# Kernel tuning notes

Measured on AMD Instinct MI355X. Metric: run time of the kernel, lower is better.

## Reference

```python
import jax, jax.numpy as jnp
import numpy as np

D_MODEL = 128
D_STATE = 16
D_CONV = 4
EXPAND = 2
D_INNER = EXPAND * D_MODEL        # 256
DT_RANK = (D_MODEL + 15) // 16    # 8


def setup_inputs() -> dict:
    key = jax.random.key(0)
    ks = jax.random.split(key, 12)
    bsz, dd, hh, ww = 2, 8, 32, 32
    x = jax.random.normal(ks[0], (bsz, D_MODEL, dd, hh, ww), dtype=jnp.float32)
    # LayerNorm params
    ln_w = jnp.ones((D_MODEL,), jnp.float32)
    ln_b = jnp.zeros((D_MODEL,), jnp.float32)
    # Mamba params (fan-in scaled random init)
    W_in = jax.random.normal(ks[1], (2 * D_INNER, D_MODEL), jnp.float32) / np.sqrt(D_MODEL)
    conv_w = jax.random.normal(ks[2], (D_INNER, D_CONV), jnp.float32) / np.sqrt(D_CONV)
    conv_b = jnp.zeros((D_INNER,), jnp.float32)
    W_x = jax.random.normal(ks[3], (DT_RANK + 2 * D_STATE, D_INNER), jnp.float32) / np.sqrt(D_INNER)
    W_dt = jax.random.normal(ks[4], (D_INNER, DT_RANK), jnp.float32) / np.sqrt(DT_RANK)
    # bias so softplus(dt) starts small, as in mamba's dt init
    b_dt = jnp.log(jnp.expm1(jax.random.uniform(ks[5], (D_INNER,), jnp.float32, 1e-3, 0.1)))
    # A_log = log(1..d_state) broadcast over channels (S4D-real init)
    A_log = jnp.log(jnp.broadcast_to(jnp.arange(1, D_STATE + 1, dtype=jnp.float32), (D_INNER, D_STATE)))
    D = jnp.ones((D_INNER,), jnp.float32)
    W_out = jax.random.normal(ks[6], (D_MODEL, D_INNER), jnp.float32) / np.sqrt(D_INNER)
    return {"x": x, "ln_w": ln_w, "ln_b": ln_b, "W_in": W_in, "conv_w": conv_w,
            "conv_b": conv_b, "W_x": W_x, "W_dt": W_dt, "b_dt": b_dt,
            "A_log": A_log, "D": D, "W_out": W_out}


def _mamba_layer(x, ln_w, ln_b, W_in, conv_w, conv_b, W_x, W_dt, b_dt, A_log, D, W_out):
    bsz, c, dd, hh, ww = x.shape
    L = dd * hh * ww
    xs = x.transpose(0, 2, 3, 4, 1).reshape(bsz, L, c)          # (b, L, d_model)
    # LayerNorm
    mu = xs.mean(-1, keepdims=True)
    var = ((xs - mu) ** 2).mean(-1, keepdims=True)
    xn = (xs - mu) * jax.lax.rsqrt(var + 1e-5) * ln_w + ln_b
    # in_proj -> x, z
    xz = jnp.einsum('blc,ec->ble', xn, W_in)                     # (b, L, 2*d_inner)
    xi, z = xz[..., :D_INNER], xz[..., D_INNER:]
    # causal depthwise conv1d + silu
    xi_t = xi.transpose(0, 2, 1)                                  # (b, d_inner, L)
    xc = jax.lax.conv_general_dilated(
        xi_t, conv_w[:, None, :], window_strides=(1,),
        padding=[(D_CONV - 1, 0)], feature_group_count=D_INNER)
    xc = jax.nn.silu(xc + conv_b[None, :, None]).transpose(0, 2, 1)  # (b, L, d_inner)
    # x_proj -> dt, B, C
    dbl = jnp.einsum('bld,ed->ble', xc, W_x)
    dt = dbl[..., :DT_RANK]
    Bm = dbl[..., DT_RANK:DT_RANK + D_STATE]                      # (b, L, n)
    Cm = dbl[..., DT_RANK + D_STATE:]                             # (b, L, n)
    dt = jax.nn.softplus(jnp.einsum('blr,dr->bld', dt, W_dt) + b_dt)  # (b, L, d_inner)
    A = -jnp.exp(A_log)                                           # (d_inner, n)
    dA = jnp.exp(jnp.einsum('bld,dn->bldn', dt, A))               # (b, L, d_inner, n)
    dBx = jnp.einsum('bln,bld->bldn', Bm, dt * xc)                # (b, L, d_inner, n)

    def step(h, inp):
        dA_t, dBx_t, C_t = inp
        h = dA_t * h + dBx_t                                      # (b, d_inner, n)
        y = jnp.einsum('bdn,bn->bd', h, C_t)
        return h, y

    h0 = jnp.zeros((bsz, D_INNER, D_STATE), xc.dtype)
    _, ys = jax.lax.scan(step, h0,
                         (dA.transpose(1, 0, 2, 3), dBx.transpose(1, 0, 2, 3), Cm.transpose(1, 0, 2)))
    y = ys.transpose(1, 0, 2) + xc * D                            # (b, L, d_inner)
    y = y * jax.nn.silu(z)
    out = jnp.einsum('bld,cd->blc', y, W_out)                     # (b, L, d_model)
    return out.reshape(bsz, dd, hh, ww, c).transpose(0, 4, 1, 2, 3)


def reference(x, ln_w, ln_b, W_in, conv_w, conv_b, W_x, W_dt, b_dt, A_log, D, W_out):
    return _mamba_layer(x, ln_w, ln_b, W_in, conv_w, conv_b, W_x, W_dt, b_dt, A_log, D, W_out)
```

## Files before the change

### kernel.cpp

```cpp
#include <hip/hip_runtime.h>

constexpr int kB  = 2;
constexpr int kL  = 8192;
constexpr int kC  = 128;
constexpr int kE  = 256;
constexpr int kN  = 16;
constexpr int kCL = 64;
constexpr int kNC = kL / kCL;

typedef __attribute__((ext_vector_type(8))) short bf16x8;
typedef __attribute__((ext_vector_type(4))) float f32x4;
typedef __attribute__((ext_vector_type(8))) unsigned short u16x8;

__device__ __forceinline__ float silu(float v) { return v / (1.f + __expf(-v)); }
__device__ __forceinline__ float softplusf(float s) {
  return fmaxf(s, 0.f) + log1pf(__expf(-fabsf(s)));
}
__device__ __forceinline__ unsigned short f2bf(float x) {
  unsigned u = __float_as_uint(x);
  u += 0x7FFF + ((u >> 16) & 1);
  return (unsigned short)(u >> 16);
}
__device__ __forceinline__ float bf2f(unsigned short x) {
  return __uint_as_float(((unsigned)x) << 16);
}
__device__ __forceinline__ float dpp_red8(float v) {
  v += __int_as_float(__builtin_amdgcn_mov_dpp(__float_as_int(v), 0xB1, 0xF, 0xF, true));
  v += __int_as_float(__builtin_amdgcn_mov_dpp(__float_as_int(v), 0x4E, 0xF, 0xF, true));
  v += __int_as_float(__builtin_amdgcn_mov_dpp(__float_as_int(v), 0x141, 0xF, 0xF, true));
  return v;
}

__global__ __launch_bounds__(256) void k_pre(const float* __restrict__ W_in,
                                             const float* __restrict__ W_x,
                                             const float* __restrict__ W_dt,
                                             const float* __restrict__ W_out,
                                             unsigned short* __restrict__ WinF,
                                             unsigned short* __restrict__ WcatF,
                                             unsigned short* __restrict__ WoutF,
                                             const float* __restrict__ x,
                                             const float* __restrict__ ln_w,
                                             const float* __restrict__ ln_b,
                                             unsigned short* __restrict__ xnH) {
  const int tid = threadIdx.x;
  if (blockIdx.x < 84) {
    const int f = blockIdx.x * 256 + tid;
    u16x8 o;
    if (f < 8192) {
      const int lane = f & 63, ks = (f >> 6) & 3, mt = f >> 8;
      const int m = mt * 16 + (lane & 15), kb = ks * 32 + ((lane >> 4) << 3);
      #pragma unroll
      for (int j = 0; j < 8; ++j) o[j] = f2bf(W_in[m * 128 + kb + j]);
      *(u16x8*)&WinF[(size_t)f * 8] = o;
    } else if (f < 17408) {
      const int g = f - 8192;
      const int lane = g & 63, ks = (g >> 6) & 7, mt = g >> 9;
      const int m = mt * 16 + (lane & 15), kb = ks * 32 + ((lane >> 4) << 3);
      if (m < 256) {
        #pragma unroll
        for (int j = 0; j < 8; ++j) {
          float s = 0.f;
          #pragma unroll
          for (int r = 0; r < 8; ++r) s = fmaf(W_dt[m * 8 + r], W_x[r * 256 + kb + j], s);
          o[j] = f2bf(s);
        }
      } else {
        #pragma unroll
        for (int j = 0; j < 8; ++j) o[j] = f2bf(W_x[(8 + m - 256) * 256 + kb + j]);
      }
      *(u16x8*)&WcatF[(size_t)g * 8] = o;
    } else {
      const int g = f - 17408;
      const int lane = g & 63, ks = (g >> 6) & 7, mt = g >> 9;
      const int m = mt * 16 + (lane & 15), kb = ks * 32 + ((lane >> 4) << 3);
      #pragma unroll
      for (int j = 0; j < 8; ++j) o[j] = f2bf(W_out[m * 256 + kb + j]);
      *(u16x8*)&WoutF[(size_t)g * 8] = o;
    }
    return;
  }
  __shared__ float tile[64 * 132];
  __shared__ float smu[64], srs[64];
  const int bx2 = blockIdx.x - 84;
  const int b = bx2 >> 7, l0 = (bx2 & 127) * 64;
  const int cc = tid >> 6, lt = tid & 63;
  const float* xb = x + (size_t)b * kC * kL;
  for (int c0 = 0; c0 < kC; c0 += 4)
    tile[lt * 132 + c0 + cc] = xb[(size_t)(c0 + cc) * kL + l0 + lt];
  __syncthreads();
  const int l = tid >> 2, q = tid & 3;
  float s = 0.f, s2 = 0.f;
  #pragma unroll
  for (int i = 0; i < 32; ++i) {
    const float v = tile[l * 132 + q + 4 * i];
    s += v; s2 += v * v;
  }
  s += __shfl_xor(s, 1);  s2 += __shfl_xor(s2, 1);
  s += __shfl_xor(s, 2);  s2 += __shfl_xor(s2, 2);
  if (q == 0) {
    const float mu = s * (1.f / 128.f);
    const float var = s2 * (1.f / 128.f) - mu * mu;
    smu[l] = mu; srs[l] = rsqrtf(var + 1e-5f);
  }
  __syncthreads();
  #pragma unroll
  for (int it = 0; it < 4; ++it) {
    const int fidx = tid + it * 256;
    const int li = fidx >> 4, c8 = fidx & 15;
    const float4 v0 = *(const float4*)&tile[li * 132 + c8 * 8];
    const float4 v1 = *(const float4*)&tile[li * 132 + c8 * 8 + 4];
    const float4 w0 = *(const float4*)&ln_w[c8 * 8];
    const float4 w1 = *(const float4*)&ln_w[c8 * 8 + 4];
    const float4 b0 = *(const float4*)&ln_b[c8 * 8];
    const float4 b1 = *(const float4*)&ln_b[c8 * 8 + 4];
    const float mu = smu[li], rs = srs[li];
    u16x8 o;
    o[0] = f2bf((v0.x - mu) * rs * w0.x + b0.x);
    o[1] = f2bf((v0.y - mu) * rs * w0.y + b0.y);
    o[2] = f2bf((v0.z - mu) * rs * w0.z + b0.z);
    o[3] = f2bf((v0.w - mu) * rs * w0.w + b0.w);
    o[4] = f2bf((v1.x - mu) * rs * w1.x + b1.x);
    o[5] = f2bf((v1.y - mu) * rs * w1.y + b1.y);
    o[6] = f2bf((v1.z - mu) * rs * w1.z + b1.z);
    o[7] = f2bf((v1.w - mu) * rs * w1.w + b1.w);
    *(u16x8*)&xnH[((size_t)b * kL + l0 + li) * kC + c8 * 8] = o;
  }
}

__global__ __launch_bounds__(256) void k_g1conv(const unsigned short* __restrict__ xnH,
                                                const unsigned short* __restrict__ WF,
                                                const float* __restrict__ W_in,
                                                const float* __restrict__ conv_w,
                                                const float* __restrict__ conv_b,
                                                float* __restrict__ zT,
                                                float* __restrict__ xcT,
                                                unsigned short* __restrict__ xcH) {
  constexpr int KPAD = 136;
  __shared__ unsigned short Xs[64 * KPAD];
  __shared__ float xi[128 * 69];
  const int b = blockIdx.z, ct = blockIdx.y, l0 = blockIdx.x * 64;
  const int tid = threadIdx.x, lane = tid & 63, w = tid >> 6;
  for (int si = tid; si < 1024; si += 256) {
    const int l = si >> 4, k8 = si & 15;
    *(uint4*)&Xs[l * KPAD + k8 * 8] =
        *(const uint4*)&xnH[((size_t)(b * kL + l0 + l)) * kC + k8 * 8];
  }
  __syncthreads();
  float s0 = 0.f, s1 = 0.f, s2 = 0.f;
  if (ct < 2 && tid < 128 && l0 > 0) {
    const int ge = ct * 128 + tid;
    const float4* wv = (const float4*)&W_in[ge * kC];
    const u16x8* x0 = (const u16x8*)&xnH[((size_t)b * kL + l0 - 3) * kC];
    const u16x8* x1 = (const u16x8*)&xnH[((size_t)b * kL + l0 - 2) * kC];
    const u16x8* x2 = (const u16x8*)&xnH[((size_t)b * kL + l0 - 1) * kC];
    #pragma unroll 4
    for (int k8 = 0; k8 < 16; ++k8) {
      const float4 wa = wv[2 * k8], wb = wv[2 * k8 + 1];
      const u16x8 a0 = x0[k8], a1 = x1[k8], a2 = x2[k8];
      const float wreg[8] = {wa.x, wa.y, wa.z, wa.w, wb.x, wb.y, wb.z, wb.w};
      #pragma unroll
      for (int j = 0; j < 8; ++j) {
        s0 = fmaf(wreg[j], bf2f(a0[j]), s0);
        s1 = fmaf(wreg[j], bf2f(a1[j]), s1);
        s2 = fmaf(wreg[j], bf2f(a2[j]), s2);
      }
    }
  }
  if (ct < 2 && tid < 128) {
    xi[tid * 69 + 0] = s0; xi[tid * 69 + 1] = s1; xi[tid * 69 + 2] = s2;
  }
  f32x4 acc[2][4];
  #pragma unroll
  for (int i = 0; i < 2; ++i)
    #pragma unroll
    for (int lt = 0; lt < 4; ++lt) acc[i][lt] = (f32x4){0.f, 0.f, 0.f, 0.f};
  const int colo = lane & 15, kgrp = (lane >> 4) * 8;
  for (int ks = 0; ks < 4; ++ks) {
    bf16x8 Bf[4];
    #pragma unroll
    for (int lt = 0; lt < 4; ++lt)
      Bf[lt] = *(const bf16x8*)&Xs[(lt * 16 + colo) * KPAD + ks * 32 + kgrp];
    #pragma unroll
    for (int i = 0; i < 2; ++i) {
      const int mt_g = ct * 8 + w + 4 * i;
      const bf16x8 Af = *(const bf16x8*)&WF[(size_t)((mt_g * 4 + ks) * 64 + lane) * 8];
      #pragma unroll
      for (int lt = 0; lt < 4; ++lt)
        acc[i][lt] = __builtin_amdgcn_mfma_f32_16x16x32_bf16(Af, Bf[lt], acc[i][lt], 0, 0, 0);
    }
  }
  if (ct >= 2) {
    #pragma unroll
    for (int i = 0; i < 2; ++i) {
      const int m = (ct * 8 + w + 4 * i) * 16 + (lane >> 4) * 4;
      #pragma unroll
      for (int r = 0; r < 4; ++r)
        #pragma unroll
        for (int lt = 0; lt < 4; ++lt)
          zT[((size_t)b * kE + m + r - 256) * kL + l0 + lt * 16 + colo] = acc[i][lt][r];
    }
    return;
  }
  #pragma unroll
  for (int i = 0; i < 2; ++i) {
    const int mloc = (w + 4 * i) * 16 + (lane >> 4) * 4;
    #pragma unroll
    for (int r = 0; r < 4; ++r)
      #pragma unroll
      for (int lt = 0; lt < 4; ++lt)
        xi[(mloc + r) * 69 + 3 + lt * 16 + colo] = acc[i][lt][r];
  }
  __syncthreads();
  unsigned short* ht = Xs;
  const int e = tid >> 2, q = tid & 3;
  #pragma unroll
  for (int half = 0; half < 2; ++half) {
    const int ee = e + 64 * half;
    const int ge = ct * 128 + ee;
    const float4 cw = ((const float4*)conv_w)[ge];
    const float cb = conv_b[ge];
    const float* xr = &xi[ee * 69 + q * 16];
    float o[16];
    #pragma unroll
    for (int j = 0; j < 16; ++j) {
      const float s = cb + cw.x * xr[j] + cw.y * xr[j + 1] + cw.z * xr[j + 2] + cw.w * xr[j + 3];
      o[j] = silu(s);
    }
    float4* dst = (float4*)&xcT[((size_t)b * kE + ge) * kL + l0 + q * 16];
    #pragma unroll
    for (int m = 0; m < 4; ++m) {
      float4 ov; ov.x = o[4 * m]; ov.y = o[4 * m + 1]; ov.z = o[4 * m + 2]; ov.w = o[4 * m + 3];
      dst[m] = ov;
    }
    u16x8 h0, h1;
    #pragma unroll
    for (int i = 0; i < 8; ++i) { h0[i] = f2bf(o[i]); h1[i] = f2bf(o[8 + i]); }
    if (half) __syncthreads();
    *(u16x8*)&ht[e * 72 + q * 16]     = h0;
    *(u16x8*)&ht[e * 72 + q * 16 + 8] = h1;
    __syncthreads();
    const int lr = tid >> 2, g = tid & 3;
    u16x8 r0, r1;
    #pragma unroll
    for (int i = 0; i < 8; ++i) {
      r0[i] = ht[(g * 16 + i) * 72 + lr];
      r1[i] = ht[(g * 16 + 8 + i) * 72 + lr];
    }
    unsigned short* orow = &xcH[((size_t)b * kL + l0 + lr) * kE + ct * 128 + half * 64 + g * 16];
    *(u16x8*)orow = r0;
    *(u16x8*)(orow + 8) = r1;
  }
}

template<int K, int M, int CT, int VARIANT>
__global__ __launch_bounds__(256) void k_mfma(const unsigned short* __restrict__ XH,
                                              const unsigned short* __restrict__ WF,
                                              const float* __restrict__ bdt,
                                              float* __restrict__ out0,
                                              float* __restrict__ out1) {
  constexpr int KS = K / 32;
  constexpr int MT_BLK = M / 16 / CT;
  constexpr int MT_W = (MT_BLK + 3) / 4;
  constexpr int KPAD = K + 8;
  __shared__ unsigned short Xs[64 * KPAD];
  const int b = blockIdx.z, ct = blockIdx.y, l0 = blockIdx.x * 64;
  const int tid = threadIdx.x, lane = tid & 63, w = tid >> 6;
  for (int si = tid; si < 64 * K / 8; si += 256) {
    const int l = si / (K / 8), k8 = si % (K / 8);
    *(uint4*)&Xs[l * KPAD + k8 * 8] =
        *(const uint4*)&XH[((size_t)(b * kL + l0 + l)) * K + k8 * 8];
  }
  __syncthreads();
  f32x4 acc[MT_W][4];
  #pragma unroll
  for (int i = 0; i < MT_W; ++i)
    #pragma unroll
    for (int lt = 0; lt < 4; ++lt) acc[i][lt] = (f32x4){0.f, 0.f, 0.f, 0.f};
  const int colo = lane & 15, kgrp = (lane >> 4) * 8;
  for (int ks = 0; ks < KS; ++ks) {
    bf16x8 Bf[4];
    #pragma unroll
    for (int lt = 0; lt < 4; ++lt)
      Bf[lt] = *(const bf16x8*)&Xs[(lt * 16 + colo) * KPAD + ks * 32 + kgrp];
    #pragma unroll
    for (int i = 0; i < MT_W; ++i) {
      const int mt = w + 4 * i;
      if (mt < MT_BLK) {
        const int mt_g = ct * MT_BLK + mt;
        const bf16x8 Af = *(const bf16x8*)&WF[(size_t)((mt_g * KS + ks) * 64 + lane) * 8];
        #pragma unroll
        for (int lt = 0; lt < 4; ++lt)
          acc[i][lt] = __builtin_amdgcn_mfma_f32_16x16x32_bf16(Af, Bf[lt], acc[i][lt], 0, 0, 0);
      }
    }
  }
  #pragma unroll
  for (int i = 0; i < MT_W; ++i) {
    const int mt = w + 4 * i;
    if (mt >= MT_BLK) continue;
    const int mbase = (ct * MT_BLK + mt) * 16 + (lane >> 4) * 4;
    #pragma unroll
    for (int r = 0; r < 4; ++r) {
      const int m = mbase + r;
      #pragma unroll
      for (int lt = 0; lt < 4; ++lt) {
        const int lg = l0 + lt * 16 + colo;
        const float v = acc[i][lt][r];
        if (VARIANT == 1) {
          if (m < 256) out0[((size_t)b * kE + m) * kL + lg] = softplusf(v + bdt[m]);
          else         out1[((size_t)b * 32 + m - 256) * kL + lg] = v;
        } else {
          out0[((size_t)b * kC + m) * kL + lg] = v;
        }
      }
    }
  }
}

__global__ __launch_bounds__(256) void k_scanA(const float* __restrict__ dtT,
                                               const float* __restrict__ xcT,
                                               const float* __restrict__ bcT,
                                               const float* __restrict__ A_log,
                                               float* __restrict__ hloc,
                                               float* __restrict__ aprod) {
  __shared__ float dxi[32 * 132];
  __shared__ float Bp[8 * 132];
  const int b = blockIdx.z, ch = blockIdx.x, d0 = blockIdx.y * 32;
  const int l0 = ch * kCL, tid = threadIdx.x;
  {
    const int ds = tid >> 3, ng = tid & 7;
    const float4* dsrc = (const float4*)&dtT[((size_t)b * kE + d0 + ds) * kL + l0 + 8 * ng];
    const float4* xsrc = (const float4*)&xcT[((size_t)b * kE + d0 + ds) * kL + l0 + 8 * ng];
    float* wr = &dxi[ds * 132 + 16 * ng];
    #pragma unroll
    for (int m = 0; m < 2; ++m) {
      const float4 dv = dsrc[m], xv = xsrc[m];
      *(float4*)&wr[8 * m]     = make_float4(dv.x, dv.x * xv.x, dv.y, dv.y * xv.y);
      *(float4*)&wr[8 * m + 4] = make_float4(dv.z, dv.z * xv.z, dv.w, dv.w * xv.w);
    }
  }
  if (tid < 128) {
    const int ng = tid & 7, lq = tid >> 3;
    const float4 b0 = *(const float4*)&bcT[((size_t)b * 32 + 2 * ng) * kL + l0 + 4 * lq];
    const float4 b1 = *(const float4*)&bcT[((size_t)b * 32 + 2 * ng + 1) * kL + l0 + 4 * lq];
    float* wr = &Bp[ng * 132 + 8 * lq];
    *(float4*)&wr[0] = make_float4(b0.x, b1.x, b0.y, b1.y);
    *(float4*)&wr[4] = make_float4(b0.z, b1.z, b0.w, b1.w);
  }
  __syncthreads();
  const int ds = tid >> 3, ng = tid & 7;
  const int d = d0 + ds;
  const float2 Al = *(const float2*)&A_log[d * kN + 2 * ng];
  const float Av0 = -__expf(Al.x), Av1 = -__expf(Al.y);
  float h0 = 0.f, h1 = 0.f, sdt = 0.f;
  const float* drow = &dxi[ds * 132];
  const float* brow = &Bp[ng * 132];
  #pragma unroll 4
  for (int l = 0; l < kCL; l += 2) {
    const float4 du = *(const float4*)&drow[2 * l];
    const float4 bb = *(const float4*)&brow[2 * l];
    sdt += du.x + du.z;
    h0 = fmaf(__expf(Av0 * du.x), h0, bb.x * du.y);
    h1 = fmaf(__expf(Av1 * du.x), h1, bb.y * du.y);
    h0 = fmaf(__expf(Av0 * du.z), h0, bb.z * du.w);
    h1 = fmaf(__expf(Av1 * du.z), h1, bb.w * du.w);
  }
  const size_t base = (((size_t)b * kNC + ch) * kE + d) * kN + 2 * ng;
  *(float2*)&hloc[base] = make_float2(h0, h1);
  *(float2*)&aprod[base] = make_float2(__expf(Av0 * sdt), __expf(Av1 * sdt));
}

__global__ __launch_bounds__(256) void k_prefix8(float* __restrict__ hs,
                                                 const float* __restrict__ aprod) {
  const int t = blockIdx.x * 256 + threadIdx.x;
  const int row = t >> 3, seg = t & 7;
  const int b = row >> 12, dn = row & 4095;
  const size_t idx0 = ((size_t)b * kNC + seg * 16) * 4096 + dn;
  float hl[16], ap[16];
  #pragma unroll
  for (int i = 0; i < 16; ++i) {
    hl[i] = hs[idx0 + (size_t)i * 4096];
    ap[i] = aprod[idx0 + (size_t)i * 4096];
  }
  float H = 0.f, A = 1.f;
  #pragma unroll
  for (int i = 0; i < 16; ++i) { H = fmaf(ap[i], H, hl[i]); A *= ap[i]; }
  #pragma unroll
  for (int off = 1; off < 8; off <<= 1) {
    const float Ho = __shfl_up(H, off, 8);
    const float Ao = __shfl_up(A, off, 8);
    if (seg >= off) { H = fmaf(A, Ho, H); A *= Ao; }
  }
  const float Hprev = __shfl_up(H, 1, 8);
  float h = (seg == 0) ? 0.f : Hprev;
  #pragma unroll
  for (int i = 0; i < 16; ++i) {
    hs[idx0 + (size_t)i * 4096] = h;
    h = fmaf(ap[i], h, hl[i]);
  }
}

__global__ __launch_bounds__(256) void k_scanC(const float* __restrict__ dtT,
                                               const float* __restrict__ xcT,
                                               const float* __restrict__ bcT,
                                               const float* __restrict__ zT,
                                               const float* __restrict__ A_log,
                                               const float* __restrict__ Dp,
                                               const float* __restrict__ hinit,
                                               unsigned short* __restrict__ yH) {
  __shared__ float dxi[32 * 132];
  __shared__ float bc4[8 * 260];
  float* yt = dxi;
  const int b = blockIdx.z, ch = blockIdx.x, d0 = blockIdx.y * 32;
  const int l0 = ch * kCL, tid = threadIdx.x;
  {
    const int ds = tid >> 3, ng = tid & 7;
    const float4* dsrc = (const float4*)&dtT[((size_t)b * kE + d0 + ds) * kL + l0 + 8 * ng];
    const float4* xsrc = (const float4*)&xcT[((size_t)b * kE + d0 + ds) * kL + l0 + 8 * ng];
    float* wr = &dxi[ds * 132 + 16 * ng];
    #pragma unroll
    for (int m = 0; m < 2; ++m) {
      const float4 dv = dsrc[m], xv = xsrc[m];
      *(float4*)&wr[8 * m]     = make_float4(dv.x, dv.x * xv.x, dv.y, dv.y * xv.y);
      *(float4*)&wr[8 * m + 4] = make_float4(dv.z, dv.z * xv.z, dv.w, dv.w * xv.w);
    }
  }
  if (tid < 128) {
    const int ng = tid & 7, lq = tid >> 3;
    const float4 b0 = *(const float4*)&bcT[((size_t)b * 32 + 2 * ng) * kL + l0 + 4 * lq];
    const float4 c0 = *(const float4*)&bcT[((size_t)b * 32 + 16 + 2 * ng) * kL + l0 + 4 * lq];
    const float4 b1 = *(const float4*)&bcT[((size_t)b * 32 + 2 * ng + 1) * kL + l0 + 4 * lq];
    const float4 c1 = *(const float4*)&bcT[((size_t)b * 32 + 17 + 2 * ng) * kL + l0 + 4 * lq];
    float* wr = &bc4[ng * 260 + 16 * lq];
    *(float4*)&wr[0]  = make_float4(b0.x, c0.x, b1.x, c1.x);
    *(float4*)&wr[4]  = make_float4(b0.y, c0.y, b1.y, c1.y);
    *(float4*)&wr[8]  = make_float4(b0.z, c0.z, b1.z, c1.z);
    *(float4*)&wr[12] = make_float4(b0.w, c0.w, b1.w, c1.w);
  }
  __syncthreads();
  const int ds = tid >> 3, ng = tid & 7;
  const int d = d0 + ds;
  const float2 Al = *(const float2*)&A_log[d * kN + 2 * ng];
  const float Av0 = -__expf(Al.x), Av1 = -__expf(Al.y);
  const size_t hbase = (((size_t)b * kNC + ch) * kE + d) * kN + 2 * ng;
  const float2 hv = *(const float2*)&hinit[hbase];
  float h0 = hv.x, h1 = hv.y;
  const float* drow = &dxi[ds * 132];
  const float* brow = &bc4[ng * 260];
  float yreg[8];
  #pragma unroll
  for (int l = 0; l < kCL; l += 2) {
    const float4 du  = *(const float4*)&drow[2 * l];
    const float4 bcA = *(const float4*)&brow[4 * l];
    const float4 bcB = *(const float4*)&brow[4 * l + 4];
    h0 = fmaf(__expf(Av0 * du.x), h0, bcA.x * du.y);
    h1 = fmaf(__expf(Av1 * du.x), h1, bcA.z * du.y);
    const float ylo = dpp_red8(fmaf(h0, bcA.y, h1 * bcA.w));
    h0 = fmaf(__expf(Av0 * du.z), h0, bcB.x * du.w);
    h1 = fmaf(__expf(Av1 * du.z), h1, bcB.z * du.w);
    const float yhi = dpp_red8(fmaf(h0, bcB.y, h1 * bcB.w));
    if (ng == (l & 7))       yreg[l >> 3] = ylo;
    if (ng == ((l + 1) & 7)) yreg[l >> 3] = yhi;
  }
  __syncthreads();
  #pragma unroll
  for (int k = 0; k < 8; ++k)
    yt[ds * 72 + 8 * k + ng] = yreg[k];
  __syncthreads();
  const int l = tid >> 2, g = tid & 3;
  u16x8 ov;
  #pragma unroll
  for (int i = 0; i < 8; ++i) {
    const int dd = g * 8 + i;
    const float yv = yt[dd * 72 + l];
    const float xv = xcT[((size_t)b * kE + d0 + dd) * kL + l0 + l];
    const float zv = zT[((size_t)b * kE + d0 + dd) * kL + l0 + l];
    const float o = fmaf(xv, Dp[d0 + dd], yv) * silu(zv);
    ov[i] = f2bf(o);
  }
  *(u16x8*)&yH[((size_t)b * kL + l0 + l) * kE + d0 + g * 8] = ov;
}

extern "C" void kernel_launch(void* const* d_in, const int* in_sizes, int n_in,
                              void* d_out, int out_size, void* d_ws, size_t ws_size,
                              hipStream_t stream) {
  (void)in_sizes; (void)n_in; (void)out_size; (void)ws_size;
  const float* x      = (const float*)d_in[0];
  const float* ln_w   = (const float*)d_in[1];
  const float* ln_b   = (const float*)d_in[2];
  const float* W_in   = (const float*)d_in[3];
  const float* conv_w = (const float*)d_in[4];
  const float* conv_b = (const float*)d_in[5];
  const float* W_x    = (const float*)d_in[6];
  const float* W_dt   = (const float*)d_in[7];
  const float* b_dt   = (const float*)d_in[8];
  const float* A_log  = (const float*)d_in[9];
  const float* Dp     = (const float*)d_in[10];
  const float* W_out  = (const float*)d_in[11];
  float* out = (float*)d_out;
  float* ws  = (float*)d_ws;

  float* zT    = ws + 4194304;
  float* xcT   = ws + 8388608;
  float* dtT   = ws + 12582912;
  float* bcT   = ws + 16777216;
  float* hloc  = ws + 17301504;
  float* aprod = ws + 18350080;
  unsigned short* xnH  = (unsigned short*)(ws + 12582912);
  unsigned short* xcH  = (unsigned short*)(ws + 17301504);
  unsigned short* yH   = (unsigned short*)(ws);
  unsigned short* WinF = (unsigned short*)(ws + 19398656);
  unsigned short* WcatF = WinF + 65536;
  unsigned short* WoutF = WinF + 139264;

  k_pre   <<<340, 256, 0, stream>>>(W_in, W_x, W_dt, W_out, WinF, WcatF, WoutF,
                                    x, ln_w, ln_b, xnH);
  k_g1conv<<<dim3(kL / 64, 4, kB), 256, 0, stream>>>(xnH, WinF, W_in, conv_w, conv_b,
                                                     zT, xcT, xcH);
  k_mfma<256, 288, 2, 1><<<dim3(kL / 64, 2, kB), 256, 0, stream>>>(xcH, WcatF, b_dt, dtT, bcT);
  k_scanA <<<dim3(kNC, kE / 32, kB), 256, 0, stream>>>(dtT, xcT, bcT, A_log, hloc, aprod);
  k_prefix8<<<256, 256, 0, stream>>>(hloc, aprod);
  k_scanC <<<dim3(kNC, kE / 32, kB), 256, 0, stream>>>(dtT, xcT, bcT, zT, A_log, Dp, hloc, yH);
  k_mfma<256, 128, 1, 2><<<dim3(kL / 64, 1, kB), 256, 0, stream>>>(yH, WoutF, nullptr, out, nullptr);
}
```

Before: 118.3 us.

## Store z, xc and B/C intermediates in bf16 and read them directly in scans

Stores the z gate, the conv output xc, and the B/C projections as bf16 instead of fp32, halving their write and read traffic. The B/C values are interleaved so the scan kernels can load them directly from global memory, which removes the shared-memory staging and block barriers in scanA and scanC. The templated GEMM is split into specialized kernels. The risk is extra rounding error in the scan inputs and less coalesced global loads inside the recurrence loop.

```diff
diff --git a/kernel.cpp b/kernel.cpp
--- a/kernel.cpp
+++ b/kernel.cpp
@@ -132,8 +132,8 @@
                                                 const float* __restrict__ W_in,
                                                 const float* __restrict__ conv_w,
                                                 const float* __restrict__ conv_b,
-                                                float* __restrict__ zT,
-                                                float* __restrict__ xcT,
+                                                unsigned short* __restrict__ zH,
+                                                unsigned short* __restrict__ xcC,
                                                 unsigned short* __restrict__ xcH) {
   constexpr int KPAD = 136;
   __shared__ unsigned short Xs[64 * KPAD];
@@ -190,14 +190,23 @@
     }
   }
   if (ct >= 2) {
+    unsigned short* ht2 = (unsigned short*)xi;
     #pragma unroll
     for (int i = 0; i < 2; ++i) {
-      const int m = (ct * 8 + w + 4 * i) * 16 + (lane >> 4) * 4;
+      const int lrow = (w + 4 * i) * 16 + (lane >> 4) * 4;
       #pragma unroll
       for (int r = 0; r < 4; ++r)
         #pragma unroll
         for (int lt = 0; lt < 4; ++lt)
-          zT[((size_t)b * kE + m + r - 256) * kL + l0 + lt * 16 + colo] = acc[i][lt][r];
+          ht2[(lrow + r) * 72 + lt * 16 + colo] = f2bf(acc[i][lt][r]);
+    }
+    __syncthreads();
+    #pragma unroll
+    for (int k = 0; k < 4; ++k) {
+      const int it = tid + k * 256;
+      const int row = it >> 3, c8 = it & 7;
+      const u16x8 v = *(const u16x8*)&ht2[row * 72 + c8 * 8];
+      *(u16x8*)&zH[((size_t)b * kE + (ct - 2) * 128 + row) * kL + l0 + c8 * 8] = v;
     }
     return;
   }
@@ -226,15 +235,12 @@
       const float s = cb + cw.x * xr[j] + cw.y * xr[j + 1] + cw.z * xr[j + 2] + cw.w * xr[j + 3];
       o[j] = silu(s);
     }
-    float4* dst = (float4*)&xcT[((size_t)b * kE + ge) * kL + l0 + q * 16];
-    #pragma unroll
-    for (int m = 0; m < 4; ++m) {
-      float4 ov; ov.x = o[4 * m]; ov.y = o[4 * m + 1]; ov.z = o[4 * m + 2]; ov.w = o[4 * m + 3];
-      dst[m] = ov;
-    }
     u16x8 h0, h1;
     #pragma unroll
     for (int i = 0; i < 8; ++i) { h0[i] = f2bf(o[i]); h1[i] = f2bf(o[8 + i]); }
+    unsigned short* crow = &xcC[((size_t)b * kE + ge) * kL + l0 + q * 16];
+    *(u16x8*)crow = h0;
+    *(u16x8*)(crow + 8) = h1;
     if (half) __syncthreads();
     *(u16x8*)&ht[e * 72 + q * 16]     = h0;
     *(u16x8*)&ht[e * 72 + q * 16 + 8] = h1;
@@ -252,42 +258,39 @@
   }
 }
 
-template<int K, int M, int CT, int VARIANT>
-__global__ __launch_bounds__(256) void k_mfma(const unsigned short* __restrict__ XH,
-                                              const unsigned short* __restrict__ WF,
-                                              const float* __restrict__ bdt,
-                                              float* __restrict__ out0,
-                                              float* __restrict__ out1) {
-  constexpr int KS = K / 32;
-  constexpr int MT_BLK = M / 16 / CT;
-  constexpr int MT_W = (MT_BLK + 3) / 4;
-  constexpr int KPAD = K + 8;
+__global__ __launch_bounds__(256) void k_dbc(const unsigned short* __restrict__ XH,
+                                             const unsigned short* __restrict__ WF,
+                                             const float* __restrict__ bdt,
+                                             float* __restrict__ dtT,
+                                             unsigned short* __restrict__ bcQ) {
+  constexpr int KPAD = 264;
   __shared__ unsigned short Xs[64 * KPAD];
+  __shared__ float bcTile[32 * 68];
   const int b = blockIdx.z, ct = blockIdx.y, l0 = blockIdx.x * 64;
   const int tid = threadIdx.x, lane = tid & 63, w = tid >> 6;
-  for (int si = tid; si < 64 * K / 8; si += 256) {
-    const int l = si / (K / 8), k8 = si % (K / 8);
+  for (int si = tid; si < 64 * 32; si += 256) {
+    const int l = si >> 5, k8 = si & 31;
     *(uint4*)&Xs[l * KPAD + k8 * 8] =
-        *(const uint4*)&XH[((size_t)(b * kL + l0 + l)) * K + k8 * 8];
-  }
-  __syncthreads();
-  f32x4 acc[MT_W][4];
-  #pragma unroll
-  for (int i = 0; i < MT_W; ++i)
+        *(const uint4*)&XH[((size_t)(b * kL + l0 + l)) * kE + k8 * 8];
+  }
+  __syncthreads();
+  f32x4 acc[3][4];
+  #pragma unroll
+  for (int i = 0; i < 3; ++i)
     #pragma unroll
     for (int lt = 0; lt < 4; ++lt) acc[i][lt] = (f32x4){0.f, 0.f, 0.f, 0.f};
   const int colo = lane & 15, kgrp = (lane >> 4) * 8;
-  for (int ks = 0; ks < KS; ++ks) {
+  for (int ks = 0; ks < 8; ++ks) {
     bf16x8 Bf[4];
     #pragma unroll
     for (int lt = 0; lt < 4; ++lt)
       Bf[lt] = *(const bf16x8*)&Xs[(lt * 16 + colo) * KPAD + ks * 32 + kgrp];
     #pragma unroll
-    for (int i = 0; i < MT_W; ++i) {
+    for (int i = 0; i < 3; ++i) {
       const int mt = w + 4 * i;
-      if (mt < MT_BLK) {
-        const int mt_g = ct * MT_BLK + mt;
-        const bf16x8 Af = *(const bf16x8*)&WF[(size_t)((mt_g * KS + ks) * 64 + lane) * 8];
+      if (mt < 9) {
+        const int mt_g = ct * 9 + mt;
+        const bf16x8 Af = *(const bf16x8*)&WF[(size_t)((mt_g * 8 + ks) * 64 + lane) * 8];
         #pragma unroll
         for (int lt = 0; lt < 4; ++lt)
           acc[i][lt] = __builtin_amdgcn_mfma_f32_16x16x32_bf16(Af, Bf[lt], acc[i][lt], 0, 0, 0);
@@ -295,75 +298,72 @@
     }
   }
   #pragma unroll
-  for (int i = 0; i < MT_W; ++i) {
+  for (int i = 0; i < 3; ++i) {
     const int mt = w + 4 * i;
-    if (mt >= MT_BLK) continue;
-    const int mbase = (ct * MT_BLK + mt) * 16 + (lane >> 4) * 4;
+    if (mt >= 9) continue;
+    const int mbase = (ct * 9 + mt) * 16 + (lane >> 4) * 4;
     #pragma unroll
     for (int r = 0; r < 4; ++r) {
       const int m = mbase + r;
       #pragma unroll
       for (int lt = 0; lt < 4; ++lt) {
-        const int lg = l0 + lt * 16 + colo;
+        const int ll = lt * 16 + colo;
         const float v = acc[i][lt][r];
-        if (VARIANT == 1) {
-          if (m < 256) out0[((size_t)b * kE + m) * kL + lg] = softplusf(v + bdt[m]);
-          else         out1[((size_t)b * 32 + m - 256) * kL + lg] = v;
-        } else {
-          out0[((size_t)b * kC + m) * kL + lg] = v;
-        }
+        if (m < 256) dtT[((size_t)b * kE + m) * kL + l0 + ll] = softplusf(v + bdt[m]);
+        else         bcTile[(m - 256) * 68 + ll] = v;
       }
     }
   }
+  if (ct == 1) {
+    __syncthreads();
+    #pragma unroll
+    for (int k = 0; k < 2; ++k) {
+      const int it = tid + k * 256;
+      const int p = it >> 6, l = it & 63;
+      ushort4 ov;
+      ov.x = f2bf(bcTile[(2 * p) * 68 + l]);
+      ov.y = f2bf(bcTile[(16 + 2 * p) * 68 + l]);
+      ov.z = f2bf(bcTile[(2 * p + 1) * 68 + l]);
+      ov.w = f2bf(bcTile[(17 + 2 * p) * 68 + l]);
+      *(ushort4*)&bcQ[(((size_t)b * 8 + p) * kL + l0 + l) * 4] = ov;
+    }
+  }
 }
 
 __global__ __launch_bounds__(256) void k_scanA(const float* __restrict__ dtT,
-                                               const float* __restrict__ xcT,
-                                               const float* __restrict__ bcT,
+                                               const unsigned short* __restrict__ xcC,
+                                               const unsigned short* __restrict__ bcQ,
                                                const float* __restrict__ A_log,
                                                float* __restrict__ hloc,
                                                float* __restrict__ aprod) {
-  __shared__ float dxi[32 * 132];
-  __shared__ float Bp[8 * 132];
   const int b = blockIdx.z, ch = blockIdx.x, d0 = blockIdx.y * 32;
   const int l0 = ch * kCL, tid = threadIdx.x;
-  {
-    const int ds = tid >> 3, ng = tid & 7;
-    const float4* dsrc = (const float4*)&dtT[((size_t)b * kE + d0 + ds) * kL + l0 + 8 * ng];
-    const float4* xsrc = (const float4*)&xcT[((size_t)b * kE + d0 + ds) * kL + l0 + 8 * ng];
-    float* wr = &dxi[ds * 132 + 16 * ng];
-    #pragma unroll
-    for (int m = 0; m < 2; ++m) {
-      const float4 dv = dsrc[m], xv = xsrc[m];
-      *(float4*)&wr[8 * m]     = make_float4(dv.x, dv.x * xv.x, dv.y, dv.y * xv.y);
-      *(float4*)&wr[8 * m + 4] = make_float4(dv.z, dv.z * xv.z, dv.w, dv.w * xv.w);
-    }
-  }
-  if (tid < 128) {
-    const int ng = tid & 7, lq = tid >> 3;
-    const float4 b0 = *(const float4*)&bcT[((size_t)b * 32 + 2 * ng) * kL + l0 + 4 * lq];
-    const float4 b1 = *(const float4*)&bcT[((size_t)b * 32 + 2 * ng + 1) * kL + l0 + 4 * lq];
-    float* wr = &Bp[ng * 132 + 8 * lq];
-    *(float4*)&wr[0] = make_float4(b0.x, b1.x, b0.y, b1.y);
-    *(float4*)&wr[4] = make_float4(b0.z, b1.z, b0.w, b1.w);
-  }
-  __syncthreads();
   const int ds = tid >> 3, ng = tid & 7;
   const int d = d0 + ds;
   const float2 Al = *(const float2*)&A_log[d * kN + 2 * ng];
   const float Av0 = -__expf(Al.x), Av1 = -__expf(Al.y);
+  const float4* dt4 = (const float4*)&dtT[((size_t)b * kE + d) * kL + l0];
+  const ushort4* xc4 = (const ushort4*)&xcC[((size_t)b * kE + d) * kL + l0];
+  const u16x8* bc8 = (const u16x8*)&bcQ[(((size_t)b * 8 + ng) * kL + l0) * 4];
   float h0 = 0.f, h1 = 0.f, sdt = 0.f;
-  const float* drow = &dxi[ds * 132];
-  const float* brow = &Bp[ng * 132];
   #pragma unroll 4
-  for (int l = 0; l < kCL; l += 2) {
-    const float4 du = *(const float4*)&drow[2 * l];
-    const float4 bb = *(const float4*)&brow[2 * l];
-    sdt += du.x + du.z;
-    h0 = fmaf(__expf(Av0 * du.x), h0, bb.x * du.y);
-    h1 = fmaf(__expf(Av1 * du.x), h1, bb.y * du.y);
-    h0 = fmaf(__expf(Av0 * du.z), h0, bb.z * du.w);
-    h1 = fmaf(__expf(Av1 * du.z), h1, bb.w * du.w);
+  for (int lq = 0; lq < 16; ++lq) {
+    const float4 dtv = dt4[lq];
+    const ushort4 xcv = xc4[lq];
+    const u16x8 bcA = bc8[2 * lq], bcB = bc8[2 * lq + 1];
+    float dtj, u;
+    dtj = dtv.x; u = dtj * bf2f(xcv.x); sdt += dtj;
+    h0 = fmaf(__expf(Av0 * dtj), h0, bf2f(bcA[0]) * u);
+    h1 = fmaf(__expf(Av1 * dtj), h1, bf2f(bcA[2]) * u);
+    dtj = dtv.y; u = dtj * bf2f(xcv.y); sdt += dtj;
+    h0 = fmaf(__expf(Av0 * dtj), h0, bf2f(bcA[4]) * u);
+    h1 = fmaf(__expf(Av1 * dtj), h1, bf2f(bcA[6]) * u);
+    dtj = dtv.z; u = dtj * bf2f(xcv.z); sdt += dtj;
+    h0 = fmaf(__expf(Av0 * dtj), h0, bf2f(bcB[0]) * u);
+    h1 = fmaf(__expf(Av1 * dtj), h1, bf2f(bcB[2]) * u);
+    dtj = dtv.w; u = dtj * bf2f(xcv.w); sdt += dtj;
+    h0 = fmaf(__expf(Av0 * dtj), h0, bf2f(bcB[4]) * u);
+    h1 = fmaf(__expf(Av1 * dtj), h1, bf2f(bcB[6]) * u);
   }
   const size_t base = (((size_t)b * kNC + ch) * kE + d) * kN + 2 * ng;
   *(float2*)&hloc[base] = make_float2(h0, h1);
@@ -401,43 +401,16 @@
 }
 
 __global__ __launch_bounds__(256) void k_scanC(const float* __restrict__ dtT,
-                                               const float* __restrict__ xcT,
-                                               const float* __restrict__ bcT,
-                                               const float* __restrict__ zT,
+                                               const unsigned short* __restrict__ xcC,
+                                               const unsigned short* __restrict__ bcQ,
+                                               const unsigned short* __restrict__ zH,
                                                const float* __restrict__ A_log,
                                                const float* __restrict__ Dp,
                                                const float* __restrict__ hinit,
                                                unsigned short* __restrict__ yH) {
-  __shared__ float dxi[32 * 132];
-  __shared__ float bc4[8 * 260];
-  float* yt = dxi;
+  __shared__ float yt[32 * 72];
   const int b = blockIdx.z, ch = blockIdx.x, d0 = blockIdx.y * 32;
   const int l0 = ch * kCL, tid = threadIdx.x;
-  {
-    const int ds = tid >> 3, ng = tid & 7;
-    const float4* dsrc = (const float4*)&dtT[((size_t)b * kE + d0 + ds) * kL + l0 + 8 * ng];
-    const float4* xsrc = (const float4*)&xcT[((size_t)b * kE + d0 + ds) * kL + l0 + 8 * ng];
-    float* wr = &dxi[ds * 132 + 16 * ng];
-    #pragma unroll
-    for (int m = 0; m < 2; ++m) {
-      const float4 dv = dsrc[m], xv = xsrc[m];
-      *(float4*)&wr[8 * m]     = make_float4(dv.x, dv.x * xv.x, dv.y, dv.y * xv.y);
-      *(float4*)&wr[8 * m + 4] = make_float4(dv.z, dv.z * xv.z, dv.w, dv.w * xv.w);
-    }
-  }
-  if (tid < 128) {
-    const int ng = tid & 7, lq = tid >> 3;
-    const float4 b0 = *(const float4*)&bcT[((size_t)b * 32 + 2 * ng) * kL + l0 + 4 * lq];
-    const float4 c0 = *(const float4*)&bcT[((size_t)b * 32 + 16 + 2 * ng) * kL + l0 + 4 * lq];
-    const float4 b1 = *(const float4*)&bcT[((size_t)b * 32 + 2 * ng + 1) * kL + l0 + 4 * lq];
-    const float4 c1 = *(const float4*)&bcT[((size_t)b * 32 + 17 + 2 * ng) * kL + l0 + 4 * lq];
-    float* wr = &bc4[ng * 260 + 16 * lq];
-    *(float4*)&wr[0]  = make_float4(b0.x, c0.x, b1.x, c1.x);
-    *(float4*)&wr[4]  = make_float4(b0.y, c0.y, b1.y, c1.y);
-    *(float4*)&wr[8]  = make_float4(b0.z, c0.z, b1.z, c1.z);
-    *(float4*)&wr[12] = make_float4(b0.w, c0.w, b1.w, c1.w);
-  }
-  __syncthreads();
   const int ds = tid >> 3, ng = tid & 7;
   const int d = d0 + ds;
   const float2 Al = *(const float2*)&A_log[d * kN + 2 * ng];
@@ -445,24 +418,29 @@
   const size_t hbase = (((size_t)b * kNC + ch) * kE + d) * kN + 2 * ng;
   const float2 hv = *(const float2*)&hinit[hbase];
   float h0 = hv.x, h1 = hv.y;
-  const float* drow = &dxi[ds * 132];
-  const float* brow = &bc4[ng * 260];
+  const float4* dt4 = (const float4*)&dtT[((size_t)b * kE + d) * kL + l0];
+  const ushort4* xc4 = (const ushort4*)&xcC[((size_t)b * kE + d) * kL + l0];
+  const u16x8* bc8 = (const u16x8*)&bcQ[(((size_t)b * 8 + ng) * kL + l0) * 4];
   float yreg[8];
   #pragma unroll
-  for (int l = 0; l < kCL; l += 2) {
-    const float4 du  = *(const float4*)&drow[2 * l];
-    const float4 bcA = *(const float4*)&brow[4 * l];
-    const float4 bcB = *(const float4*)&brow[4 * l + 4];
-    h0 = fmaf(__expf(Av0 * du.x), h0, bcA.x * du.y);
-    h1 = fmaf(__expf(Av1 * du.x), h1, bcA.z * du.y);
-    const float ylo = dpp_red8(fmaf(h0, bcA.y, h1 * bcA.w));
-    h0 = fmaf(__expf(Av0 * du.z), h0, bcB.x * du.w);
-    h1 = fmaf(__expf(Av1 * du.z), h1, bcB.z * du.w);
-    const float yhi = dpp_red8(fmaf(h0, bcB.y, h1 * bcB.w));
-    if (ng == (l & 7))       yreg[l >> 3] = ylo;
-    if (ng == ((l + 1) & 7)) yreg[l >> 3] = yhi;
-  }
-  __syncthreads();
+  for (int lq = 0; lq < 16; ++lq) {
+    const float4 dtv = dt4[lq];
+    const ushort4 xcv = xc4[lq];
+    const u16x8 bcA = bc8[2 * lq], bcB = bc8[2 * lq + 1];
+    const float dts[4] = {dtv.x, dtv.y, dtv.z, dtv.w};
+    const float xcs[4] = {bf2f(xcv.x), bf2f(xcv.y), bf2f(xcv.z), bf2f(xcv.w)};
+    #pragma unroll
+    for (int j = 0; j < 4; ++j) {
+      const int l = 4 * lq + j;
+      const u16x8& bb = (j < 2) ? bcA : bcB;
+      const int o4 = (j & 1) * 4;
+      const float dtj = dts[j], u = dtj * xcs[j];
+      h0 = fmaf(__expf(Av0 * dtj), h0, bf2f(bb[o4 + 0]) * u);
+      h1 = fmaf(__expf(Av1 * dtj), h1, bf2f(bb[o4 + 2]) * u);
+      const float yp = dpp_red8(fmaf(h0, bf2f(bb[o4 + 1]), h1 * bf2f(bb[o4 + 3])));
+      if (ng == (l & 7)) yreg[l >> 3] = yp;
+    }
+  }
   #pragma unroll
   for (int k = 0; k < 8; ++k)
     yt[ds * 72 + 8 * k + ng] = yreg[k];
@@ -473,12 +451,56 @@
   for (int i = 0; i < 8; ++i) {
     const int dd = g * 8 + i;
     const float yv = yt[dd * 72 + l];
-    const float xv = xcT[((size_t)b * kE + d0 + dd) * kL + l0 + l];
-    const float zv = zT[((size_t)b * kE + d0 + dd) * kL + l0 + l];
+    const float xv = bf2f(xcC[((size_t)b * kE + d0 + dd) * kL + l0 + l]);
+    const float zv = bf2f(zH[((size_t)b * kE + d0 + dd) * kL + l0 + l]);
     const float o = fmaf(xv, Dp[d0 + dd], yv) * silu(zv);
     ov[i] = f2bf(o);
   }
   *(u16x8*)&yH[((size_t)b * kL + l0 + l) * kE + d0 + g * 8] = ov;
+}
+
+__global__ __launch_bounds__(256) void k_gemm3(const unsigned short* __restrict__ XH,
+                                               const unsigned short* __restrict__ WF,
+                                               float* __restrict__ out) {
+  constexpr int KPAD = 264;
+  __shared__ unsigned short Xs[64 * KPAD];
+  const int b = blockIdx.z, l0 = blockIdx.x * 64;
+  const int tid = threadIdx.x, lane = tid & 63, w = tid >> 6;
+  for (int si = tid; si < 64 * 32; si += 256) {
+    const int l = si >> 5, k8 = si & 31;
+    *(uint4*)&Xs[l * KPAD + k8 * 8] =
+        *(const uint4*)&XH[((size_t)(b * kL + l0 + l)) * kE + k8 * 8];
+  }
+  __syncthreads();
+  f32x4 acc[2][4];
+  #pragma unroll
+  for (int i = 0; i < 2; ++i)
+    #pragma unroll
+    for (int lt = 0; lt < 4; ++lt) acc[i][lt] = (f32x4){0.f, 0.f, 0.f, 0.f};
+  const int colo = lane & 15, kgrp = (lane >> 4) * 8;
+  for (int ks = 0; ks < 8; ++ks) {
+    bf16x8 Bf[4];
+    #pragma unroll
+    for (int lt = 0; lt < 4; ++lt)
+      Bf[lt] = *(const bf16x8*)&Xs[(lt * 16 + colo) * KPAD + ks * 32 + kgrp];
+    #pragma unroll
+    for (int i = 0; i < 2; ++i) {
+      const int mt = w + 4 * i;
+      const bf16x8 Af = *(const bf16x8*)&WF[(size_t)((mt * 8 + ks) * 64 + lane) * 8];
+      #pragma unroll
+      for (int lt = 0; lt < 4; ++lt)
+        acc[i][lt] = __builtin_amdgcn_mfma_f32_16x16x32_bf16(Af, Bf[lt], acc[i][lt], 0, 0, 0);
+    }
+  }
+  #pragma unroll
+  for (int i = 0; i < 2; ++i) {
+    const int mbase = (w + 4 * i) * 16 + (lane >> 4) * 4;
+    #pragma unroll
+    for (int r = 0; r < 4; ++r)
+      #pragma unroll
+      for (int lt = 0; lt < 4; ++lt)
+        out[((size_t)b * kC + mbase + r) * kL + l0 + lt * 16 + colo] = acc[i][lt][r];
+  }
 }
 
 extern "C" void kernel_launch(void* const* d_in, const int* in_sizes, int n_in,
@@ -500,15 +522,15 @@
   float* out = (float*)d_out;
   float* ws  = (float*)d_ws;
 
-  float* zT    = ws + 4194304;
-  float* xcT   = ws + 8388608;
+  unsigned short* yH  = (unsigned short*)(ws);
+  unsigned short* zH  = (unsigned short*)(ws + 4194304);
+  unsigned short* xcC = (unsigned short*)(ws + 6291456);
+  unsigned short* xcH = (unsigned short*)(ws + 8388608);
   float* dtT   = ws + 12582912;
-  float* bcT   = ws + 16777216;
+  unsigned short* bcQ = (unsigned short*)(ws + 16777216);
   float* hloc  = ws + 17301504;
   float* aprod = ws + 18350080;
   unsigned short* xnH  = (unsigned short*)(ws + 12582912);
-  unsigned short* xcH  = (unsigned short*)(ws + 17301504);
-  unsigned short* yH   = (unsigned short*)(ws);
   unsigned short* WinF = (unsigned short*)(ws + 19398656);
   unsigned short* WcatF = WinF + 65536;
   unsigned short* WoutF = WinF + 139264;
@@ -516,10 +538,10 @@
   k_pre   <<<340, 256, 0, stream>>>(W_in, W_x, W_dt, W_out, WinF, WcatF, WoutF,
                                     x, ln_w, ln_b, xnH);
   k_g1conv<<<dim3(kL / 64, 4, kB), 256, 0, stream>>>(xnH, WinF, W_in, conv_w, conv_b,
-                                                     zT, xcT, xcH);
-  k_mfma<256, 288, 2, 1><<<dim3(kL / 64, 2, kB), 256, 0, stream>>>(xcH, WcatF, b_dt, dtT, bcT);
-  k_scanA <<<dim3(kNC, kE / 32, kB), 256, 0, stream>>>(dtT, xcT, bcT, A_log, hloc, aprod);
+                                                     zH, xcC, xcH);
+  k_dbc   <<<dim3(kL / 64, 2, kB), 256, 0, stream>>>(xcH, WcatF, b_dt, dtT, bcQ);
+  k_scanA <<<dim3(kNC, kE / 32, kB), 256, 0, stream>>>(dtT, xcC, bcQ, A_log, hloc, aprod);
   k_prefix8<<<256, 256, 0, stream>>>(hloc, aprod);
-  k_scanC <<<dim3(kNC, kE / 32, kB), 256, 0, stream>>>(dtT, xcT, bcT, zT, A_log, Dp, hloc, yH);
-  k_mfma<256, 128, 1, 2><<<dim3(kL / 64, 1, kB), 256, 0, stream>>>(yH, WoutF, nullptr, out, nullptr);
-}
+  k_scanC <<<dim3(kNC, kE / 32, kB), 256, 0, stream>>>(dtT, xcC, bcQ, zH, A_log, Dp, hloc, yH);
+  k_gemm3 <<<dim3(kL / 64, 1, kB), 256, 0, stream>>>(yH, WoutF, out);
+}
```

After: 145.9 us. 23.3% more time.
